# Kernel tuning notes

Hardware: AMD Instinct MI355X
Metric: run time of the kernel (lower is better)

## Reference

```python
import jax, jax.numpy as jnp
import numpy as np
from jax import lax
import math

B, CH, BINS, CROP = 8, 2, 1024, 1024
NUM_BANDS = 4
FF = 2048
EPS = 1e-5
SCALE = 0.02  # weight init scale for numeric stability


def _inorm(x, g, b):
    # InstanceNorm2d: x [B, C, H, W], normalize over (H, W) per (B, C); biased var
    m = x.mean(axis=(2, 3), keepdims=True)
    v = x.var(axis=(2, 3), keepdims=True)
    return (x - m) / jnp.sqrt(v + EPS) * g[None, :, None, None] + b[None, :, None, None]


def _dwconv(x, k):
    # depthwise conv1d: x [B, bins, W], k [bins, 1, 3], padding=1, groups=bins
    return lax.conv_general_dilated(x, k, (1,), [(1, 1)],
                                    dimension_numbers=('NCH', 'OIH', 'NCH'),
                                    feature_group_count=x.shape[1])


def setup_inputs() -> dict:
    key = jax.random.key(0)
    ks = jax.random.split(key, 12)
    inp = {
        'x': jax.random.normal(ks[0], (B, CH, BINS, CROP), jnp.float32),
        'prev_qk': jax.random.normal(ks[1], (B, NUM_BANDS, CROP, CROP), jnp.float32),
        'g_in': jnp.ones((CROP,), jnp.float32),
        'b_in': jnp.zeros((CROP,), jnp.float32),
        'W_in': jax.random.normal(ks[2], (1, CH), jnp.float32) * SCALE,
        'bias_in': jnp.zeros((1,), jnp.float32),
        'g1': jnp.ones((CROP,), jnp.float32),
        'b1': jnp.zeros((CROP,), jnp.float32),
        'Wq': jax.random.normal(ks[3], (BINS, BINS), jnp.float32) * SCALE,
        'Wk': jax.random.normal(ks[4], (BINS, BINS), jnp.float32) * SCALE,
        'Wv': jax.random.normal(ks[5], (BINS, BINS), jnp.float32) * SCALE,
        'Wo': jax.random.normal(ks[6], (BINS, BINS), jnp.float32) * SCALE,
        'kq': jax.random.normal(ks[7], (BINS, 1, 3), jnp.float32) * SCALE,
        'kk': jax.random.normal(ks[8], (BINS, 1, 3), jnp.float32) * SCALE,
        'kv': jax.random.normal(ks[9], (BINS, 1, 3), jnp.float32) * SCALE,
        'pos_w': jax.random.normal(ks[10], (BINS // NUM_BANDS, CROP), jnp.float32) * SCALE,
        'g2': jnp.ones((CROP,), jnp.float32),
        'b2': jnp.zeros((CROP,), jnp.float32),
        'W_ff': jax.random.normal(ks[11], (1, 2), jnp.float32) * SCALE,
        'bias_ff': jnp.zeros((1,), jnp.float32),
        'W1': jax.random.normal(jax.random.fold_in(key, 100), (FF, BINS), jnp.float32) * SCALE,
        'W2': jax.random.normal(jax.random.fold_in(key, 101), (BINS, FF), jnp.float32) * SCALE,
    }
    return inp


def reference(x, prev_qk, g_in, b_in, W_in, bias_in, g1, b1, Wq, Wk, Wv, Wo,
              kq, kk, kv, pos_w, g2, b2, W_ff, bias_ff, W1, W2):
    b = x.shape[0]
    nb = NUM_BANDS
    hd = BINS // nb
    # in_norm + in_project: transposed layout [B, CROP, BINS, CH]
    xt = jnp.transpose(x, (0, 3, 2, 1))
    xt = _inorm(xt, g_in, b_in)
    xt = jnp.einsum('bwhc,oc->bwho', xt, W_in) + bias_in  # [B,CROP,BINS,1]
    x0 = jnp.transpose(xt, (0, 3, 2, 1))                  # [B,1,BINS,CROP]
    # norm1 + attention over frames (w == CROP, c == BINS)
    h = jnp.transpose(_inorm(jnp.transpose(x0, (0, 3, 2, 1)), g1, b1), (0, 3, 2, 1))
    a_in = jnp.transpose(h, (0, 3, 2, 1))[..., 0]         # [B, W, BINS]
    q = jnp.einsum('bwc,oc->bwo', a_in, Wq)
    q = jnp.transpose(_dwconv(jnp.transpose(q, (0, 2, 1)), kq), (0, 2, 1))
    k = jnp.einsum('bwc,oc->bwo', a_in, Wk)
    k = jnp.transpose(_dwconv(jnp.transpose(k, (0, 2, 1)), kk), (0, 2, 1))
    v = jnp.einsum('bwc,oc->bwo', a_in, Wv)
    v = jnp.transpose(_dwconv(jnp.transpose(v, (0, 2, 1)), kv), (0, 2, 1))
    q4 = jnp.transpose(q.reshape(b, CROP, nb, hd), (0, 2, 1, 3))   # [B,nb,W,hd]
    k4 = jnp.transpose(k.reshape(b, CROP, nb, hd), (0, 2, 3, 1))   # [B,nb,hd,W]
    v4 = jnp.transpose(v.reshape(b, CROP, nb, hd), (0, 2, 1, 3))   # [B,nb,W,hd]
    # relative-position bias via pad-and-shift
    p = jnp.matmul(q4, pos_w)                                      # [B,nb,W,CROP]
    p = jnp.pad(p, ((0, 0), (0, 0), (0, 0), (1, 0)))
    p = jnp.swapaxes(p, 2, 3)[:, :, 1:, :]                         # [B,nb,CROP,W]
    qk = (jnp.matmul(q4, k4) + p) / math.sqrt(BINS)
    qk = qk + prev_qk
    a = jax.nn.softmax(qk, axis=-1)
    o = jnp.transpose(jnp.matmul(a, v4), (0, 2, 1, 3)).reshape(b, CROP, BINS)
    o = jnp.einsum('bwc,oc->bwo', o, Wo)                           # [B,W,BINS]
    h4 = jnp.transpose(o[..., None], (0, 3, 2, 1))                 # [B,1,BINS,CROP]
    x1 = jnp.concatenate([x0, h4], axis=1)                         # [B,2,BINS,CROP]
    # norm2 + ff_project + squared-ReLU FFN
    hn = _inorm(jnp.transpose(x1, (0, 3, 2, 1)), g2, b2)           # [B,CROP,BINS,2]
    hn = jnp.einsum('bwhc,oc->bwho', hn, W_ff) + bias_ff           # [B,CROP,BINS,1]
    hn = jnp.transpose(hn, (0, 3, 2, 1))                           # [B,1,BINS,CROP]
    ht = jnp.swapaxes(hn, 2, 3)                                    # [B,1,CROP,BINS]
    ht = jnp.square(jax.nn.relu(jnp.einsum('bowc,fc->bowf', ht, W1)))
    ht = jnp.einsum('bowf,cf->bowc', ht, W2)
    hf = jnp.swapaxes(ht, 2, 3)                                    # [B,1,BINS,CROP]
    out = jnp.concatenate([x1, hf], axis=1)                        # [B,3,BINS,CROP]
    return out, qk
```

## Files before the change

### kernel.cpp

```cpp
#include <hip/hip_runtime.h>
#include <stdint.h>

#define DEVI __device__ __forceinline__

typedef __attribute__((ext_vector_type(8))) short bf16x8;
typedef __attribute__((ext_vector_type(4))) float f32x4;

#define B_    8
#define CROP_ 1024
#define BINS_ 1024
#define NB_   4
#define HD_   256
#define FF_   2048
#define EPSF  1e-5f
#define OUT0_ELEMS (8ull*3ull*1024ull*1024ull)
#define MBYTE (1024ull*1024ull)
#define M1ELEM (1024ll*1024ll)

DEVI unsigned short f2bf(float f) {
  unsigned u = __builtin_bit_cast(unsigned, f);
  u += 0x7fffu + ((u >> 16) & 1u);
  return (unsigned short)(u >> 16);
}
DEVI float bf2f(unsigned short h) {
  unsigned u = ((unsigned)h) << 16;
  return __builtin_bit_cast(float, u);
}

DEVI void gload16(const unsigned short* g, unsigned short* l) {
  __builtin_amdgcn_global_load_lds(
      (const __attribute__((address_space(1))) unsigned int*)g,
      (__attribute__((address_space(3))) unsigned int*)l, 16, 0, 0);
}

DEVI void stage32(const unsigned short* g, unsigned short* lds, int ld, int k0) {
  int t = threadIdx.x;
  int wv = t >> 6, ln = t & 63;
  int srow = wv*32 + (ln >> 2);
  int scol = (ln & 3)*8;
  const unsigned short* gp = g + (size_t)srow*ld + k0 + scol;
  gload16(gp, lds + wv*32*32);
  gload16(gp + (size_t)16*ld, lds + (wv*32 + 16)*32);
}

__global__ __launch_bounds__(256) void k_conv_all(
    const float* __restrict__ Wq, const float* __restrict__ Wk,
    const float* __restrict__ Wv, const float* __restrict__ Wo,
    const float* __restrict__ W1, const float* __restrict__ W2,
    const float* __restrict__ pw,
    unsigned short* __restrict__ WQKVB, unsigned short* __restrict__ WOB,
    unsigned short* __restrict__ W1B, unsigned short* __restrict__ W2B,
    unsigned short* __restrict__ PWT) {
  long long i = (long long)blockIdx.x*256 + threadIdx.x;
  long long stride = (long long)gridDim.x*256;
  const long long total = 8*M1ELEM + (1 << 18);
  for (; i < total; i += stride) {
    if (i < 3*M1ELEM) {
      const float* s = i < M1ELEM ? Wq : (i < 2*M1ELEM ? Wk : Wv);
      WQKVB[i] = f2bf(s[i & (M1ELEM-1)]);
    } else if (i < 4*M1ELEM) { WOB[i-3*M1ELEM] = f2bf(Wo[i-3*M1ELEM]); }
    else if (i < 6*M1ELEM)   { W1B[i-4*M1ELEM] = f2bf(W1[i-4*M1ELEM]); }
    else if (i < 8*M1ELEM)   { W2B[i-6*M1ELEM] = f2bf(W2[i-6*M1ELEM]); }
    else {
      long long j = i - 8*M1ELEM;
      int w = (int)(j >> 8), d = (int)(j & 255);
      PWT[j] = f2bf(pw[d*1024 + w]);
    }
  }
}

__global__ __launch_bounds__(256) void k_instat(const float* __restrict__ x,
                                                float* __restrict__ mean, float* __restrict__ rstd) {
  int b = blockIdx.y, w0 = blockIdx.x*32;
  int t = threadIdx.x, wl = t & 31, p = t >> 5;
  const float* xb = x + (size_t)b*2*BINS_*CROP_ + w0 + wl;
  float s = 0.f, ss = 0.f;
  for (int i = p*256; i < p*256 + 256; ++i) {
    float v = xb[(size_t)i*CROP_];
    s += v; ss += v*v;
  }
  __shared__ float ls[8][32], lss[8][32];
  ls[p][wl] = s; lss[p][wl] = ss;
  __syncthreads();
  if (t < 32) {
    float S = 0.f, SS = 0.f;
    for (int q = 0; q < 8; ++q) { S += ls[q][t]; SS += lss[q][t]; }
    float m = S*(1.f/2048.f);
    float var = SS*(1.f/2048.f) - m*m;
    mean[b*CROP_ + w0 + t] = m;
    rstd[b*CROP_ + w0 + t] = rsqrtf(var + EPSF);
  }
}

__global__ __launch_bounds__(256) void k_x0(const float* __restrict__ x,
    const float* __restrict__ mean, const float* __restrict__ rstd,
    const float* __restrict__ g_in, const float* __restrict__ b_in,
    const float* __restrict__ W_in, const float* __restrict__ bias_in,
    float* __restrict__ outp, float* __restrict__ x0t) {
  int b = blockIdx.z;
  int h0 = blockIdx.y*32, w0 = blockIdx.x*32;
  int tx = threadIdx.x, ty = threadIdx.y;
  float W0 = W_in[0], W1 = W_in[1], bi = bias_in[0];
  float sW = W0 + W1;
  __shared__ float tile[32][33];
  int w = w0 + tx;
  float m = mean[b*CROP_ + w], r = rstd[b*CROP_ + w];
  float coef = r * g_in[w];
  float add = b_in[w]*sW + bi;
  for (int s = 0; s < 4; ++s) {
    int h = h0 + ty + s*8;
    size_t i0 = (((size_t)b*2)*BINS_ + h)*CROP_ + w;
    float v0 = x[i0], v1 = x[i0 + (size_t)BINS_*CROP_];
    float val = coef*(W0*v0 + W1*v1 - m*sW) + add;
    outp[(((size_t)b*3)*BINS_ + h)*CROP_ + w] = val;
    tile[ty + s*8][tx] = val;
  }
  __syncthreads();
  for (int s = 0; s < 4; ++s) {
    int wl = ty + s*8;
    x0t[((size_t)b*CROP_ + w0 + wl)*BINS_ + h0 + tx] = tile[tx][wl];
  }
}

__global__ __launch_bounds__(256) void k_norm1(const float* __restrict__ x0t,
    const float* __restrict__ g1, const float* __restrict__ b1,
    unsigned short* __restrict__ ain) {
  int r = blockIdx.x;
  int w = r & (CROP_ - 1);
  int t = threadIdx.x;
  const float* row = x0t + (size_t)r*BINS_;
  float v[4], s = 0.f, ss = 0.f;
  for (int q = 0; q < 4; ++q) { v[q] = row[t + q*256]; s += v[q]; ss += v[q]*v[q]; }
  for (int off = 32; off; off >>= 1) { s += __shfl_xor(s, off); ss += __shfl_xor(ss, off); }
  __shared__ float red[8];
  int wv = t >> 6;
  if ((t & 63) == 0) { red[wv] = s; red[4 + wv] = ss; }
  __syncthreads();
  s = red[0] + red[1] + red[2] + red[3];
  ss = red[4] + red[5] + red[6] + red[7];
  float m = s*(1.f/1024.f);
  float var = ss*(1.f/1024.f) - m*m;
  float rs = rsqrtf(var + EPSF);
  float g = g1[w], bb = b1[w];
  for (int q = 0; q < 4; ++q)
    ain[(size_t)r*BINS_ + t + q*256] = f2bf((v[q] - m)*rs*g + bb);
}

__global__ __launch_bounds__(256) void k_norm2(const float* __restrict__ x0t,
    const float* __restrict__ o2,
    const float* __restrict__ g2, const float* __restrict__ b2,
    const float* __restrict__ W_ff, const float* __restrict__ bias_ff,
    unsigned short* __restrict__ hn) {
  int r = blockIdx.x;
  int w = r & (CROP_ - 1);
  int t = threadIdx.x;
  const float* ra = x0t + (size_t)r*BINS_;
  const float* rb = o2 + (size_t)r*BINS_;
  float va[4], vb[4], s = 0.f, ss = 0.f;
  for (int q = 0; q < 4; ++q) {
    va[q] = ra[t + q*256]; vb[q] = rb[t + q*256];
    s += va[q] + vb[q]; ss += va[q]*va[q] + vb[q]*vb[q];
  }
  for (int off = 32; off; off >>= 1) { s += __shfl_xor(s, off); ss += __shfl_xor(ss, off); }
  __shared__ float red[8];
  int wv = t >> 6;
  if ((t & 63) == 0) { red[wv] = s; red[4 + wv] = ss; }
  __syncthreads();
  s = red[0] + red[1] + red[2] + red[3];
  ss = red[4] + red[5] + red[6] + red[7];
  float m = s*(1.f/2048.f);
  float var = ss*(1.f/2048.f) - m*m;
  float rs = rsqrtf(var + EPSF);
  float W0 = W_ff[0], W1f = W_ff[1];
  float gg = g2[w]*rs;
  float add = b2[w]*(W0 + W1f) + bias_ff[0];
  for (int q = 0; q < 4; ++q)
    hn[(size_t)r*BINS_ + t + q*256] = f2bf(gg*(W0*(va[q] - m) + W1f*(vb[q] - m)) + add);
}

__global__ __launch_bounds__(256) void k_dwconv(const unsigned short* __restrict__ qkvb,
    const float* __restrict__ kq, const float* __restrict__ kk2, const float* __restrict__ kv,
    unsigned short* __restrict__ qkvc) {
  int w = blockIdx.x, b = blockIdx.y, which = blockIdx.z;
  int t = threadIdx.x;
  const float* kw = which == 0 ? kq : (which == 1 ? kk2 : kv);
  const unsigned short* r0 = qkvb + (size_t)which*8*M1ELEM + ((size_t)b*CROP_ + w)*BINS_;
  unsigned short* d0 = qkvc + (size_t)which*8*M1ELEM + ((size_t)b*CROP_ + w)*BINS_;
  for (int q = 0; q < 4; ++q) {
    int c = t + q*256;
    float k0 = kw[c*3], k1 = kw[c*3 + 1], k2 = kw[c*3 + 2];
    float acc = bf2f(r0[c]) * k1;
    if (w > 0)        acc += bf2f(r0[c - BINS_]) * k0;
    if (w < CROP_-1)  acc += bf2f(r0[c + BINS_]) * k2;
    d0[c] = f2bf(acc);
  }
}

__global__ __launch_bounds__(256) void k_tr_bf16(const unsigned short* __restrict__ src,
                                                 unsigned short* __restrict__ dst) {
  int b = blockIdx.z;
  int w0 = blockIdx.x*32, c0 = blockIdx.y*32;
  int tx = threadIdx.x, ty = threadIdx.y;
  __shared__ unsigned short tile[32][33];
  const unsigned short* S = src + (size_t)b*BINS_*CROP_;
  unsigned short* D = dst + (size_t)b*BINS_*CROP_;
  for (int s = 0; s < 4; ++s)
    tile[ty + s*8][tx] = S[(size_t)(w0 + ty + s*8)*BINS_ + c0 + tx];
  __syncthreads();
  for (int s = 0; s < 4; ++s)
    D[(size_t)(c0 + ty + s*8)*CROP_ + w0 + tx] = tile[tx][ty + s*8];
}

__global__ __launch_bounds__(256) void k_tr_f32_out(const float* __restrict__ src,
                                                    float* __restrict__ outp, int ch) {
  int b = blockIdx.z;
  int w0 = blockIdx.x*32, h0 = blockIdx.y*32;
  int tx = threadIdx.x, ty = threadIdx.y;
  __shared__ float tile[32][33];
  const float* S = src + (size_t)b*CROP_*BINS_;
  for (int s = 0; s < 4; ++s)
    tile[ty + s*8][tx] = S[(size_t)(w0 + ty + s*8)*BINS_ + h0 + tx];
  __syncthreads();
  float* D = outp + (((size_t)b*3 + ch)*BINS_)*CROP_;
  for (int s = 0; s < 4; ++s)
    D[(size_t)(h0 + ty + s*8)*CROP_ + w0 + tx] = tile[tx][ty + s*8];
}

template<int MODE>
__global__ __launch_bounds__(256) void k_gemm(
    const unsigned short* __restrict__ A, int lda,
    const unsigned short* __restrict__ Bt, int ldb,
    void* __restrict__ C, int ldc, int K)
{
  __shared__ __align__(16) unsigned short lA[2*128*32];
  __shared__ __align__(16) unsigned short lB[2*128*32];
  const unsigned short* Ab = A + (size_t)blockIdx.x*128*lda;
  const unsigned short* Bb = Bt + (size_t)blockIdx.y*128*ldb;
  const int t = threadIdx.x;
  const int wv = t >> 6, ln = t & 63;
  const int wr = (wv >> 1)*64, wc = (wv & 1)*64;
  const int lr = ln & 15, lk = ln >> 4;
  f32x4 acc[4][4] = {};
  for (int k0 = 0; k0 < K; k0 += 64) {
    stage32(Ab, lA, lda, k0);
    stage32(Ab, lA + 4096, lda, k0 + 32);
    stage32(Bb, lB, ldb, k0);
    stage32(Bb, lB + 4096, ldb, k0 + 32);
    __syncthreads();
#pragma unroll
    for (int kk = 0; kk < 2; ++kk) {
      bf16x8 af[4], bfr[4];
#pragma unroll
      for (int mi = 0; mi < 4; ++mi) af[mi]  = *(const bf16x8*)&lA[kk*4096 + (wr + mi*16 + lr)*32 + lk*8];
#pragma unroll
      for (int ni = 0; ni < 4; ++ni) bfr[ni] = *(const bf16x8*)&lB[kk*4096 + (wc + ni*16 + lr)*32 + lk*8];
#pragma unroll
      for (int mi = 0; mi < 4; ++mi)
#pragma unroll
        for (int ni = 0; ni < 4; ++ni)
          acc[mi][ni] = __builtin_amdgcn_mfma_f32_16x16x32_bf16(af[mi], bfr[ni], acc[mi][ni], 0, 0, 0);
    }
    __syncthreads();
  }
  const int row0 = blockIdx.x*128 + wr + lk*4;
  const int col0 = blockIdx.y*128 + wc + lr;
#pragma unroll
  for (int mi = 0; mi < 4; ++mi)
#pragma unroll
    for (int ni = 0; ni < 4; ++ni)
#pragma unroll
      for (int j = 0; j < 4; ++j) {
        int row = row0 + mi*16 + j;
        int col = col0 + ni*16;
        float v = acc[mi][ni][j];
        if (MODE == 0) {
          ((float*)C)[(size_t)row*ldc + col] = v;
        } else if (MODE == 2) {
          float rr = fmaxf(v, 0.f);
          ((unsigned short*)C)[(size_t)row*ldc + col] = f2bf(rr*rr);
        } else {
          ((unsigned short*)C)[(size_t)(col >> 10)*8*M1ELEM + (size_t)row*1024 + (col & 1023)] = f2bf(v);
        }
      }
}

__global__ __launch_bounds__(256) void k_qkpos(
    const unsigned short* __restrict__ qc, const unsigned short* __restrict__ kc,
    const unsigned short* __restrict__ pwt,
    const float* __restrict__ prev, float* __restrict__ qkout,
    float* __restrict__ Mg, float* __restrict__ Lg)
{
  __shared__ __align__(16) unsigned short lA1[128*32], lB1[128*32], lA2[128*32], lB2[128*32];
  const int z = blockIdx.z, b = z >> 2, n = z & 3;
  const size_t bandoff = (size_t)b*CROP_*BINS_ + (size_t)n*HD_;
  const unsigned short* A1 = qc + bandoff + (size_t)blockIdx.x*128*BINS_;
  const unsigned short* B1 = kc + bandoff + (size_t)blockIdx.y*128*BINS_;
  const unsigned short* A2 = pwt + (size_t)blockIdx.x*128*HD_;
  const unsigned short* B2 = qc + bandoff + (size_t)blockIdx.y*128*BINS_;
  const int t = threadIdx.x;
  const int wv = t >> 6, ln = t & 63;
  const int wr = (wv >> 1)*64, wc = (wv & 1)*64;
  const int lr = ln & 15, lk = ln >> 4;
  f32x4 acc[4][4] = {};
  for (int k0 = 0; k0 < HD_; k0 += 32) {
    stage32(A1, lA1, BINS_, k0);
    stage32(B1, lB1, BINS_, k0);
    stage32(A2, lA2, HD_, k0);
    stage32(B2, lB2, BINS_, k0);
    __syncthreads();
    bf16x8 af[4], bfr[4];
#pragma unroll
    for (int mi = 0; mi < 4; ++mi) af[mi]  = *(const bf16x8*)&lA1[(wr + mi*16 + lr)*32 + lk*8];
#pragma unroll
    for (int ni = 0; ni < 4; ++ni) bfr[ni] = *(const bf16x8*)&lB1[(wc + ni*16 + lr)*32 + lk*8];
#pragma unroll
    for (int mi = 0; mi < 4; ++mi)
#pragma unroll
      for (int ni = 0; ni < 4; ++ni)
        acc[mi][ni] = __builtin_amdgcn_mfma_f32_16x16x32_bf16(af[mi], bfr[ni], acc[mi][ni], 0, 0, 0);
#pragma unroll
    for (int mi = 0; mi < 4; ++mi) af[mi]  = *(const bf16x8*)&lA2[(wr + mi*16 + lr)*32 + lk*8];
#pragma unroll
    for (int ni = 0; ni < 4; ++ni) bfr[ni] = *(const bf16x8*)&lB2[(wc + ni*16 + lr)*32 + lk*8];
#pragma unroll
    for (int mi = 0; mi < 4; ++mi)
#pragma unroll
      for (int ni = 0; ni < 4; ++ni)
        acc[mi][ni] = __builtin_amdgcn_mfma_f32_16x16x32_bf16(af[mi], bfr[ni], acc[mi][ni], 0, 0, 0);
    __syncthreads();
  }
  const float* pz = prev + (size_t)z*CROP_*CROP_;
  float* oz = qkout + (size_t)z*CROP_*CROP_;
  const int row0 = blockIdx.x*128 + wr + lk*4;
  const int col0 = blockIdx.y*128 + wc + lr;
  float* smf = (float*)lA1;
  float* slf = smf + 256;
  const int wch = wv & 1;
  const int rbase = wr + lk*4;
#pragma unroll
  for (int mi = 0; mi < 4; ++mi) {
    float v[4][4];
    float tmax[4];
#pragma unroll
    for (int j = 0; j < 4; ++j) tmax[j] = -1e30f;
#pragma unroll
    for (int ni = 0; ni < 4; ++ni)
#pragma unroll
      for (int j = 0; j < 4; ++j) {
        size_t idx = (size_t)(row0 + mi*16 + j)*CROP_ + col0 + ni*16;
        float val = acc[mi][ni][j]*0.03125f + pz[idx];
        oz[idx] = val;
        v[j][ni] = val;
        tmax[j] = fmaxf(tmax[j], val);
      }
#pragma unroll
    for (int off = 1; off < 16; off <<= 1)
#pragma unroll
      for (int j = 0; j < 4; ++j) tmax[j] = fmaxf(tmax[j], __shfl_xor(tmax[j], off));
    if ((ln & 15) == 0)
#pragma unroll
      for (int j = 0; j < 4; ++j) smf[wch*128 + rbase + mi*16 + j] = tmax[j];
    __syncthreads();
    float mrow[4], psum[4];
#pragma unroll
    for (int j = 0; j < 4; ++j) {
      int rl = rbase + mi*16 + j;
      mrow[j] = fmaxf(smf[rl], smf[128 + rl]);
      psum[j] = 0.f;
#pragma unroll
      for (int ni = 0; ni < 4; ++ni) psum[j] += __expf(v[j][ni] - mrow[j]);
    }
#pragma unroll
    for (int off = 1; off < 16; off <<= 1)
#pragma unroll
      for (int j = 0; j < 4; ++j) psum[j] += __shfl_xor(psum[j], off);
    if ((ln & 15) == 0)
#pragma unroll
      for (int j = 0; j < 4; ++j) slf[wch*128 + rbase + mi*16 + j] = psum[j];
    __syncthreads();
    if (wch == 0 && (ln & 15) == 0) {
#pragma unroll
      for (int j = 0; j < 4; ++j) {
        int rl = rbase + mi*16 + j;
        int rg = blockIdx.x*128 + rl;
        size_t si = ((size_t)z*CROP_ + rg)*8 + blockIdx.y;
        Mg[si] = mrow[j];
        Lg[si] = slf[rl] + slf[128 + rl];
      }
    }
  }
}

__global__ __launch_bounds__(256) void k_mred(const float* __restrict__ Mg,
    const float* __restrict__ Lg, float* __restrict__ MF, float* __restrict__ LF) {
  int r = blockIdx.x*256 + threadIdx.x;
  float m = -1e30f;
#pragma unroll
  for (int cb = 0; cb < 8; ++cb) m = fmaxf(m, Mg[(size_t)r*8 + cb]);
  float l = 0.f;
#pragma unroll
  for (int cb = 0; cb < 8; ++cb) l += Lg[(size_t)r*8 + cb]*__expf(Mg[(size_t)r*8 + cb] - m);
  MF[r] = m;
  LF[r] = 1.f / l;
}

__global__ __launch_bounds__(256) void k_pv(
    const float* __restrict__ qk, const float* __restrict__ MF, const float* __restrict__ LF,
    const unsigned short* __restrict__ vct, unsigned short* __restrict__ ob)
{
  __shared__ __align__(16) unsigned short lA[2*128*32];
  __shared__ __align__(16) unsigned short lB[2*128*32];
  __shared__ float s_m[128];
  const int z = blockIdx.z, b = z >> 2, band = z & 3;
  const int row0 = blockIdx.x*128;
  const int cy = blockIdx.y;
  const float* qkf = qk + (size_t)z*CROP_*CROP_ + (size_t)row0*CROP_;
  const unsigned short* Bb = vct + ((size_t)b*CROP_ + band*HD_ + cy*128)*CROP_;
  const int t = threadIdx.x;
  const int wv = t >> 6, ln = t & 63;
  const int wr = (wv >> 1)*64, wc = (wv & 1)*64;
  const int lr = ln & 15, lk = ln >> 4;
  if (t < 128) s_m[t] = MF[(size_t)z*CROP_ + row0 + t];
  __syncthreads();
  f32x4 acc[4][4] = {};
  for (int k0 = 0; k0 < CROP_; k0 += 64) {
#pragma unroll
    for (int chunk = 0; chunk < 2; ++chunk) {
#pragma unroll
      for (int i = 0; i < 4; ++i) {
        int idx = i*256 + t;
        int row = idx >> 3, f4 = idx & 7;
        const float4 vv = *(const float4*)&qkf[(size_t)row*CROP_ + k0 + chunk*32 + f4*4];
        float mr = s_m[row];
        unsigned lo = (unsigned)f2bf(__expf(vv.x - mr)) | ((unsigned)f2bf(__expf(vv.y - mr)) << 16);
        unsigned hi = (unsigned)f2bf(__expf(vv.z - mr)) | ((unsigned)f2bf(__expf(vv.w - mr)) << 16);
        *(uint2*)&lA[chunk*4096 + row*32 + f4*4] = make_uint2(lo, hi);
      }
    }
    stage32(Bb, lB, CROP_, k0);
    stage32(Bb, lB + 4096, CROP_, k0 + 32);
    __syncthreads();
#pragma unroll
    for (int kk = 0; kk < 2; ++kk) {
      bf16x8 af[4], bfr[4];
#pragma unroll
      for (int mi = 0; mi < 4; ++mi) af[mi]  = *(const bf16x8*)&lA[kk*4096 + (wr + mi*16 + lr)*32 + lk*8];
#pragma unroll
      for (int ni = 0; ni < 4; ++ni) bfr[ni] = *(const bf16x8*)&lB[kk*4096 + (wc + ni*16 + lr)*32 + lk*8];
#pragma unroll
      for (int mi = 0; mi < 4; ++mi)
#pragma unroll
        for (int ni = 0; ni < 4; ++ni)
          acc[mi][ni] = __builtin_amdgcn_mfma_f32_16x16x32_bf16(af[mi], bfr[ni], acc[mi][ni], 0, 0, 0);
    }
    __syncthreads();
  }
#pragma unroll
  for (int mi = 0; mi < 4; ++mi)
#pragma unroll
    for (int j = 0; j < 4; ++j) {
      int rl = wr + lk*4 + mi*16 + j;
      float il = LF[(size_t)z*CROP_ + row0 + rl];
#pragma unroll
      for (int ni = 0; ni < 4; ++ni) {
        int col = band*HD_ + cy*128 + wc + ni*16 + lr;
        ob[((size_t)b*CROP_ + row0 + rl)*BINS_ + col] = f2bf(acc[mi][ni][j]*il);
      }
    }
}

extern "C" void kernel_launch(void* const* d_in, const int* in_sizes, int n_in,
                              void* d_out, int out_size, void* d_ws, size_t ws_size,
                              hipStream_t stream) {
  (void)in_sizes; (void)n_in; (void)out_size; (void)ws_size;
  const float* x       = (const float*)d_in[0];
  const float* prev_qk = (const float*)d_in[1];
  const float* g_in    = (const float*)d_in[2];
  const float* b_in    = (const float*)d_in[3];
  const float* W_in    = (const float*)d_in[4];
  const float* bias_in = (const float*)d_in[5];
  const float* g1      = (const float*)d_in[6];
  const float* b1      = (const float*)d_in[7];
  const float* Wq      = (const float*)d_in[8];
  const float* Wk      = (const float*)d_in[9];
  const float* Wv      = (const float*)d_in[10];
  const float* Wo      = (const float*)d_in[11];
  const float* kq      = (const float*)d_in[12];
  const float* kk      = (const float*)d_in[13];
  const float* kv      = (const float*)d_in[14];
  const float* pos_w   = (const float*)d_in[15];
  const float* g2      = (const float*)d_in[16];
  const float* b2      = (const float*)d_in[17];
  const float* W_ff    = (const float*)d_in[18];
  const float* bias_ff = (const float*)d_in[19];
  const float* W1      = (const float*)d_in[20];
  const float* W2      = (const float*)d_in[21];

  char* ws = (char*)d_ws;
  unsigned short* WQKVB = (unsigned short*)(ws + 0*MBYTE);
  unsigned short* WOB   = (unsigned short*)(ws + 6*MBYTE);
  unsigned short* W1B   = (unsigned short*)(ws + 8*MBYTE);
  unsigned short* W2B   = (unsigned short*)(ws + 12*MBYTE);
  unsigned short* PWT   = (unsigned short*)(ws + 16*MBYTE);
  float*          SMEAN = (float*)(ws + 16*MBYTE + 512*1024);
  float*          SRSTD = (float*)(ws + 16*MBYTE + 512*1024 + 32*1024);
  float*          Mg    = (float*)(ws + 17*MBYTE);
  float*          Lg    = (float*)(ws + 18*MBYTE);
  float*          MF    = (float*)(ws + 19*MBYTE);
  float*          LF    = (float*)(ws + 19*MBYTE + 256*1024);
  float*          X0T   = (float*)(ws + 20*MBYTE);
  unsigned short* AIN   = (unsigned short*)(ws + 52*MBYTE);
  unsigned short* QKVB  = (unsigned short*)(ws + 68*MBYTE);
  unsigned short* QKVC  = (unsigned short*)(ws + 116*MBYTE);
  unsigned short* VCT   = (unsigned short*)(ws + 164*MBYTE);
  unsigned short* OB    = (unsigned short*)(ws + 68*MBYTE);
  float*          O2    = (float*)(ws + 116*MBYTE);
  unsigned short* HN    = (unsigned short*)(ws + 148*MBYTE);
  unsigned short* HT    = (unsigned short*)(ws + 20*MBYTE);
  float*          HT2   = (float*)(ws + 52*MBYTE);

  float* outp  = (float*)d_out;
  float* qkout = outp + OUT0_ELEMS;

  dim3 blk256(256, 1, 1);
  dim3 blk32x8(32, 8, 1);

  k_conv_all<<<8448, blk256, 0, stream>>>(Wq, Wk, Wv, Wo, W1, W2, pos_w,
                                          WQKVB, WOB, W1B, W2B, PWT);
  k_instat<<<dim3(32, 8, 1), blk256, 0, stream>>>(x, SMEAN, SRSTD);
  k_x0<<<dim3(32, 32, 8), blk32x8, 0, stream>>>(x, SMEAN, SRSTD, g_in, b_in, W_in, bias_in, outp, X0T);
  k_norm1<<<8192, blk256, 0, stream>>>(X0T, g1, b1, AIN);
  k_gemm<5><<<dim3(64, 24, 1), blk256, 0, stream>>>(AIN, 1024, WQKVB, 1024, QKVB, 0, 1024);
  k_dwconv<<<dim3(1024, 8, 3), blk256, 0, stream>>>(QKVB, kq, kk, kv, QKVC);
  k_tr_bf16<<<dim3(32, 32, 8), blk32x8, 0, stream>>>(QKVC + (size_t)2*8*M1ELEM, VCT);
  k_qkpos<<<dim3(8, 8, 32), blk256, 0, stream>>>(QKVC, QKVC + (size_t)8*M1ELEM, PWT,
                                                 prev_qk, qkout, Mg, Lg);
  k_mred<<<128, blk256, 0, stream>>>(Mg, Lg, MF, LF);
  k_pv<<<dim3(8, 2, 32), blk256, 0, stream>>>(qkout, MF, LF, VCT, OB);
  k_gemm<0><<<dim3(64, 8, 1), blk256, 0, stream>>>(OB, 1024, WOB, 1024, O2, 1024, 1024);
  k_tr_f32_out<<<dim3(32, 32, 8), blk32x8, 0, stream>>>(O2, outp, 1);
  k_norm2<<<8192, blk256, 0, stream>>>(X0T, O2, g2, b2, W_ff, bias_ff, HN);
  k_gemm<2><<<dim3(64, 16, 1), blk256, 0, stream>>>(HN, 1024, W1B, 1024, HT, 2048, 1024);
  k_gemm<0><<<dim3(64, 8, 1), blk256, 0, stream>>>(HT, 2048, W2B, 2048, HT2, 1024, 2048);
  k_tr_f32_out<<<dim3(32, 32, 8), blk32x8, 0, stream>>>(HT2, outp, 2);
}
```

Measured before the change: 529.1 us.

## Replace GEMM with triple-buffered async-load 256x128 tile kernel; fold mred into pv

Swaps the synchronous 128x128 GEMM for a 512-thread kernel with 256x128 tiles. It streams K-tiles into three XOR-swizzled LDS buffers through direct global-to-LDS loads, using explicit vmcnt waits, barriers and raised priority around the MFMA block. This aims to overlap memory latency with matrix work and remove bank conflicts. The separate row max/sum reduction kernel is dropped and its work is done at the start of each PV block, saving a launch at the cost of redundant reductions across column blocks. The hand-written waitcnt logic is fragile and the larger LDS footprint may lower occupancy.

Measured after the change: 503.0 us. 4.9% less time.

```diff
diff --git a/kernel.cpp b/kernel.cpp
--- a/kernel.cpp
+++ b/kernel.cpp
@@ -226,44 +226,88 @@
     D[(size_t)(h0 + ty + s*8)*CROP_ + w0 + tx] = tile[tx][ty + s*8];
 }
 
+#define BUFB 49152
+#define ABYTES 32768
+
+DEVI void stage_ab(const unsigned short* Ab, int lda, const unsigned short* Bb, int ldb,
+                   int k0, unsigned short* buf, int t, int wv) {
+  int trow = t >> 3;
+  int colel = ((t & 7) ^ (trow & 7)) << 3;
+  unsigned short* lbase = buf + wv*512;
+  const unsigned short* ga = Ab + (size_t)trow*lda + k0 + colel;
+#pragma unroll
+  for (int c = 0; c < 4; ++c)
+    gload16(ga + (size_t)(c*64)*lda, lbase + c*4096);
+  const unsigned short* gb = Bb + (size_t)trow*ldb + k0 + colel;
+  unsigned short* lbb = buf + 16384 + wv*512;
+#pragma unroll
+  for (int c = 0; c < 2; ++c)
+    gload16(gb + (size_t)(c*64)*ldb, lbb + c*4096);
+}
+
 template<int MODE>
-__global__ __launch_bounds__(256) void k_gemm(
+__global__ __launch_bounds__(512) void k_gemm3(
     const unsigned short* __restrict__ A, int lda,
     const unsigned short* __restrict__ Bt, int ldb,
     void* __restrict__ C, int ldc, int K)
 {
-  __shared__ __align__(16) unsigned short lA[2*128*32];
-  __shared__ __align__(16) unsigned short lB[2*128*32];
-  const unsigned short* Ab = A + (size_t)blockIdx.x*128*lda;
+  __shared__ __align__(16) unsigned short lds[3*24576];
+  const unsigned short* Ab = A + (size_t)blockIdx.x*256*lda;
   const unsigned short* Bb = Bt + (size_t)blockIdx.y*128*ldb;
   const int t = threadIdx.x;
   const int wv = t >> 6, ln = t & 63;
-  const int wr = (wv >> 1)*64, wc = (wv & 1)*64;
+  const int wm = wv >> 1, wn = wv & 1;
   const int lr = ln & 15, lk = ln >> 4;
+  const int sx = (lr & 7) << 4;
+  const int NT = K >> 6;
+  stage_ab(Ab, lda, Bb, ldb, 0,   lds,           t, wv);
+  stage_ab(Ab, lda, Bb, ldb, 64,  lds + 24576,   t, wv);
+  stage_ab(Ab, lda, Bb, ldb, 128, lds + 49152,   t, wv);
+  asm volatile("s_waitcnt vmcnt(12)" ::: "memory");
+  __builtin_amdgcn_s_barrier();
+
   f32x4 acc[4][4] = {};
-  for (int k0 = 0; k0 < K; k0 += 64) {
-    stage32(Ab, lA, lda, k0);
-    stage32(Ab, lA + 4096, lda, k0 + 32);
-    stage32(Bb, lB, ldb, k0);
-    stage32(Bb, lB + 4096, ldb, k0 + 32);
-    __syncthreads();
+  for (int kt = 0; kt < NT; ++kt) {
+    const int cur = kt % 3;
+    const char* bufc = (const char*)lds + cur*BUFB;
+    bf16x8 af[2][4], bf[2][4];
 #pragma unroll
     for (int kk = 0; kk < 2; ++kk) {
-      bf16x8 af[4], bfr[4];
-#pragma unroll
-      for (int mi = 0; mi < 4; ++mi) af[mi]  = *(const bf16x8*)&lA[kk*4096 + (wr + mi*16 + lr)*32 + lk*8];
-#pragma unroll
-      for (int ni = 0; ni < 4; ++ni) bfr[ni] = *(const bf16x8*)&lB[kk*4096 + (wc + ni*16 + lr)*32 + lk*8];
+#pragma unroll
+      for (int mi = 0; mi < 4; ++mi) {
+        int row = wm*64 + mi*16 + lr;
+        af[kk][mi] = *(const bf16x8*)(bufc + ((row*128 + kk*64 + lk*16) ^ sx));
+      }
+#pragma unroll
+      for (int ni = 0; ni < 4; ++ni) {
+        int row = wn*64 + ni*16 + lr;
+        bf[kk][ni] = *(const bf16x8*)(bufc + ABYTES + ((row*128 + kk*64 + lk*16) ^ sx));
+      }
+    }
+    asm volatile("s_waitcnt lgkmcnt(0)" ::: "memory");
+    __builtin_amdgcn_s_barrier();
+    if (kt + 3 < NT)
+      stage_ab(Ab, lda, Bb, ldb, (kt+3)*64, (unsigned short*)((char*)lds + cur*BUFB), t, wv);
+    __builtin_amdgcn_s_setprio(1);
+#pragma unroll
+    for (int kk = 0; kk < 2; ++kk)
 #pragma unroll
       for (int mi = 0; mi < 4; ++mi)
 #pragma unroll
         for (int ni = 0; ni < 4; ++ni)
-          acc[mi][ni] = __builtin_amdgcn_mfma_f32_16x16x32_bf16(af[mi], bfr[ni], acc[mi][ni], 0, 0, 0);
-    }
-    __syncthreads();
-  }
-  const int row0 = blockIdx.x*128 + wr + lk*4;
-  const int col0 = blockIdx.y*128 + wc + lr;
+          acc[mi][ni] = __builtin_amdgcn_mfma_f32_16x16x32_bf16(af[kk][mi], bf[kk][ni], acc[mi][ni], 0, 0, 0);
+    __builtin_amdgcn_s_setprio(0);
+    if (kt + 1 < NT) {
+      int rem = (NT-1 < kt+3 ? NT-1 : kt+3) - (kt+1);
+      if (rem >= 2)      asm volatile("s_waitcnt vmcnt(12)" ::: "memory");
+      else if (rem == 1) asm volatile("s_waitcnt vmcnt(6)"  ::: "memory");
+      else               asm volatile("s_waitcnt vmcnt(0)"  ::: "memory");
+      __builtin_amdgcn_s_barrier();
+    }
+  }
+
+  const int row0 = blockIdx.x*256 + wm*64 + lk*4;
+  const int col0 = blockIdx.y*128 + wn*64 + lr;
 #pragma unroll
   for (int mi = 0; mi < 4; ++mi)
 #pragma unroll
@@ -391,26 +435,13 @@
   }
 }
 
-__global__ __launch_bounds__(256) void k_mred(const float* __restrict__ Mg,
-    const float* __restrict__ Lg, float* __restrict__ MF, float* __restrict__ LF) {
-  int r = blockIdx.x*256 + threadIdx.x;
-  float m = -1e30f;
-#pragma unroll
-  for (int cb = 0; cb < 8; ++cb) m = fmaxf(m, Mg[(size_t)r*8 + cb]);
-  float l = 0.f;
-#pragma unroll
-  for (int cb = 0; cb < 8; ++cb) l += Lg[(size_t)r*8 + cb]*__expf(Mg[(size_t)r*8 + cb] - m);
-  MF[r] = m;
-  LF[r] = 1.f / l;
-}
-
 __global__ __launch_bounds__(256) void k_pv(
-    const float* __restrict__ qk, const float* __restrict__ MF, const float* __restrict__ LF,
+    const float* __restrict__ qk, const float* __restrict__ Mg, const float* __restrict__ Lg,
     const unsigned short* __restrict__ vct, unsigned short* __restrict__ ob)
 {
   __shared__ __align__(16) unsigned short lA[2*128*32];
   __shared__ __align__(16) unsigned short lB[2*128*32];
-  __shared__ float s_m[128];
+  __shared__ float s_m[128], s_il[128];
   const int z = blockIdx.z, b = z >> 2, band = z & 3;
   const int row0 = blockIdx.x*128;
   const int cy = blockIdx.y;
@@ -420,7 +451,17 @@
   const int wv = t >> 6, ln = t & 63;
   const int wr = (wv >> 1)*64, wc = (wv & 1)*64;
   const int lr = ln & 15, lk = ln >> 4;
-  if (t < 128) s_m[t] = MF[(size_t)z*CROP_ + row0 + t];
+  if (t < 128) {
+    size_t rg = (size_t)z*CROP_ + row0 + t;
+    float m = -1e30f;
+#pragma unroll
+    for (int cb = 0; cb < 8; ++cb) m = fmaxf(m, Mg[rg*8 + cb]);
+    float l = 0.f;
+#pragma unroll
+    for (int cb = 0; cb < 8; ++cb) l += Lg[rg*8 + cb]*__expf(Mg[rg*8 + cb] - m);
+    s_m[t] = m;
+    s_il[t] = 1.f / l;
+  }
   __syncthreads();
   f32x4 acc[4][4] = {};
   for (int k0 = 0; k0 < CROP_; k0 += 64) {
@@ -460,7 +501,7 @@
 #pragma unroll
     for (int j = 0; j < 4; ++j) {
       int rl = wr + lk*4 + mi*16 + j;
-      float il = LF[(size_t)z*CROP_ + row0 + rl];
+      float il = s_il[rl];
 #pragma unroll
       for (int ni = 0; ni < 4; ++ni) {
         int col = band*HD_ + cy*128 + wc + ni*16 + lr;
@@ -506,8 +547,6 @@
   float*          SRSTD = (float*)(ws + 16*MBYTE + 512*1024 + 32*1024);
   float*          Mg    = (float*)(ws + 17*MBYTE);
   float*          Lg    = (float*)(ws + 18*MBYTE);
-  float*          MF    = (float*)(ws + 19*MBYTE);
-  float*          LF    = (float*)(ws + 19*MBYTE + 256*1024);
   float*          X0T   = (float*)(ws + 20*MBYTE);
   unsigned short* AIN   = (unsigned short*)(ws + 52*MBYTE);
   unsigned short* QKVB  = (unsigned short*)(ws + 68*MBYTE);
@@ -523,6 +562,7 @@
   float* qkout = outp + OUT0_ELEMS;
 
   dim3 blk256(256, 1, 1);
+  dim3 blk512(512, 1, 1);
   dim3 blk32x8(32, 8, 1);
 
   k_conv_all<<<8448, blk256, 0, stream>>>(Wq, Wk, Wv, Wo, W1, W2, pos_w,
@@ -530,17 +570,16 @@
   k_instat<<<dim3(32, 8, 1), blk256, 0, stream>>>(x, SMEAN, SRSTD);
   k_x0<<<dim3(32, 32, 8), blk32x8, 0, stream>>>(x, SMEAN, SRSTD, g_in, b_in, W_in, bias_in, outp, X0T);
   k_norm1<<<8192, blk256, 0, stream>>>(X0T, g1, b1, AIN);
-  k_gemm<5><<<dim3(64, 24, 1), blk256, 0, stream>>>(AIN, 1024, WQKVB, 1024, QKVB, 0, 1024);
+  k_gemm3<5><<<dim3(32, 24, 1), blk512, 0, stream>>>(AIN, 1024, WQKVB, 1024, QKVB, 0, 1024);
   k_dwconv<<<dim3(1024, 8, 3), blk256, 0, stream>>>(QKVB, kq, kk, kv, QKVC);
   k_tr_bf16<<<dim3(32, 32, 8), blk32x8, 0, stream>>>(QKVC + (size_t)2*8*M1ELEM, VCT);
   k_qkpos<<<dim3(8, 8, 32), blk256, 0, stream>>>(QKVC, QKVC + (size_t)8*M1ELEM, PWT,
                                                  prev_qk, qkout, Mg, Lg);
-  k_mred<<<128, blk256, 0, stream>>>(Mg, Lg, MF, LF);
-  k_pv<<<dim3(8, 2, 32), blk256, 0, stream>>>(qkout, MF, LF, VCT, OB);
-  k_gemm<0><<<dim3(64, 8, 1), blk256, 0, stream>>>(OB, 1024, WOB, 1024, O2, 1024, 1024);
+  k_pv<<<dim3(8, 2, 32), blk256, 0, stream>>>(qkout, Mg, Lg, VCT, OB);
+  k_gemm3<0><<<dim3(32, 8, 1), blk512, 0, stream>>>(OB, 1024, WOB, 1024, O2, 1024, 1024);
   k_tr_f32_out<<<dim3(32, 32, 8), blk32x8, 0, stream>>>(O2, outp, 1);
   k_norm2<<<8192, blk256, 0, stream>>>(X0T, O2, g2, b2, W_ff, bias_ff, HN);
-  k_gemm<2><<<dim3(64, 16, 1), blk256, 0, stream>>>(HN, 1024, W1B, 1024, HT, 2048, 1024);
-  k_gemm<0><<<dim3(64, 8, 1), blk256, 0, stream>>>(HT, 2048, W2B, 2048, HT2, 1024, 2048);
+  k_gemm3<2><<<dim3(32, 16, 1), blk512, 0, stream>>>(HN, 1024, W1B, 1024, HT, 2048, 1024);
+  k_gemm3<0><<<dim3(32, 8, 1), blk512, 0, stream>>>(HT, 2048, W2B, 2048, HT2, 1024, 2048);
   k_tr_f32_out<<<dim3(32, 32, 8), blk32x8, 0, stream>>>(HT2, outp, 2);
 }
```
